# Kernel tuning notes

Measured on AMD Instinct MI355X. Metric: run time of the kernel, lower is better.

Reference implementation:

```python
import jax, jax.numpy as jnp
import numpy as np

N, E, FIN, H, FO = 50000, 800000, 256, 8, 32


def setup_inputs() -> dict:
    key = jax.random.key(0)
    ks = jax.random.split(key, 7)
    node_features = jax.random.normal(ks[0], (N, FIN), dtype=jnp.float32)
    edge_index = jax.random.randint(ks[1], (2, E), 0, N, dtype=jnp.int32).astype(jnp.int64)
    # parameters (xavier-ish scaling)
    Wp = jax.random.normal(ks[2], (H * FO, FIN), dtype=jnp.float32) * (1.0 / np.sqrt(FIN))
    a_src = jax.random.normal(ks[3], (1, H, FO), dtype=jnp.float32) * 0.1
    a_trg = jax.random.normal(ks[4], (1, H, FO), dtype=jnp.float32) * 0.1
    Wskip = jax.random.normal(ks[5], (H * FO, FIN), dtype=jnp.float32) * (1.0 / np.sqrt(FIN))
    bias = jnp.zeros((H * FO,), dtype=jnp.float32)
    return {"node_features": node_features, "edge_index": edge_index,
            "Wp": Wp, "a_src": a_src, "a_trg": a_trg, "Wskip": Wskip, "bias": bias}


def reference(node_features, edge_index, Wp, a_src, a_trg, Wskip, bias):
    # dropout is identity at inference
    x = node_features                                   # [N, FIN]
    src, trg = edge_index[0], edge_index[1]             # [E], [E]
    proj = (x @ Wp.T).reshape(-1, H, FO)                # [N, H, FO]
    scores_src = jnp.sum(proj * a_src, axis=-1)         # [N, H]
    scores_trg = jnp.sum(proj * a_trg, axis=-1)         # [N, H]
    # lift to edges
    s = scores_src[src] + scores_trg[trg]               # [E, H]
    s = jax.nn.leaky_relu(s, negative_slope=0.2)
    # global max subtraction (matches torch code: scores.max())
    s = s - jnp.max(s)
    exp_s = jnp.exp(s)                                  # [E, H]
    denom = jax.ops.segment_sum(exp_s, trg, num_segments=N)   # [N, H]
    attn = exp_s / (denom[trg] + 1e-16)                 # [E, H]
    weighted = proj[src] * attn[:, :, None]             # [E, H, FO]
    out = jax.ops.segment_sum(weighted, trg, num_segments=N)  # [N, H, FO]
    # skip connection: FO != FIN, so use skip_proj
    out = out + (x @ Wskip.T).reshape(-1, H, FO)
    out = out.reshape(-1, H * FO) + bias                # concat heads
    return jax.nn.elu(out)
```

## Files before the change

### kernel.cpp

```cpp
#include <hip/hip_runtime.h>
#include <math.h>

#define FIN 256
#define HF  256
#define NH  8

typedef __bf16 bf16x8 __attribute__((ext_vector_type(8)));
typedef float  f32x4  __attribute__((ext_vector_type(4)));

__device__ __forceinline__ unsigned short f2bf(float f) {
    unsigned u = __float_as_uint(f);
    unsigned r = (u + 0x7fffu + ((u >> 16) & 1u)) >> 16;
    return (unsigned short)r;
}
__device__ __forceinline__ float bf2f(unsigned short h) {
    return __uint_as_float(((unsigned)h) << 16);
}

__global__ __launch_bounds__(256) void convert_k(
    const float* __restrict__ x, const float* __restrict__ Wp,
    const float* __restrict__ Wskip, unsigned short* __restrict__ A2,
    unsigned short* __restrict__ W2, int M)
{
    const int l = threadIdx.x & 63;
    const int row = blockIdx.x * 4 + (threadIdx.x >> 6);
    const int total = M + 512;
    if (row >= total) return;
    const float* src;
    unsigned short* dst;
    if (row < M) { src = x + (size_t)row * 256; dst = A2 + (size_t)row * 512; }
    else {
        int j = row - M;
        src = (j < 256) ? Wp + (size_t)j * 256 : Wskip + (size_t)(j - 256) * 256;
        dst = W2 + (size_t)j * 512;
    }
    float4 v = *(const float4*)&src[l * 4];
    ushort4 h, lo;
    h.x = f2bf(v.x); lo.x = f2bf(v.x - bf2f(h.x));
    h.y = f2bf(v.y); lo.y = f2bf(v.y - bf2f(h.y));
    h.z = f2bf(v.z); lo.z = f2bf(v.z - bf2f(h.z));
    h.w = f2bf(v.w); lo.w = f2bf(v.w - bf2f(h.w));
    *(ushort4*)&dst[l * 4]       = h;
    *(ushort4*)&dst[256 + l * 4] = lo;
}

__device__ __forceinline__ void gload16(const void* g, void* l) {
    __builtin_amdgcn_global_load_lds(
        (const __attribute__((address_space(1))) void*)g,
        (__attribute__((address_space(3))) void*)l, 16, 0, 0);
}

__global__ __launch_bounds__(256) void mfma_gemm(
    const unsigned short* __restrict__ A2, const unsigned short* __restrict__ W2,
    const float* __restrict__ bias, float* __restrict__ proj,
    float* __restrict__ out, int M)
{
    __shared__ __align__(16) unsigned short sAh[8192], sAl[8192], sBh[8192], sBl[8192];

    const int tid = threadIdx.x;
    const int l   = tid & 63;
    const int w   = tid >> 6;
    const int wr  = w >> 1, wc = w & 1;
    const int brow = blockIdx.x * 128;
    const int bcol = blockIdx.y * 128;

    f32x4 acc[4][4];
    #pragma unroll
    for (int a = 0; a < 4; ++a)
        #pragma unroll
        for (int b = 0; b < 4; ++b) acc[a][b] = (f32x4){0.f, 0.f, 0.f, 0.f};

    const int srow = l >> 3;
    const int sseg = (l & 7) ^ srow;

    for (int kk = 0; kk < 4; ++kk) {
        #pragma unroll
        for (int i = 0; i < 4; ++i) {
            const int rl  = w * 32 + i * 8 + srow;
            const int lds = (w * 32 + i * 8) * 64;
            int ga = brow + rl; if (ga >= M) ga = M - 1;
            const unsigned short* gA = A2 + (size_t)ga * 512 + kk * 64 + sseg * 8;
            const unsigned short* gB = W2 + (size_t)(bcol + rl) * 512 + kk * 64 + sseg * 8;
            gload16(gA,       &sAh[lds]);
            gload16(gA + 256, &sAl[lds]);
            gload16(gB,       &sBh[lds]);
            gload16(gB + 256, &sBl[lds]);
        }
        __syncthreads();

        #pragma unroll
        for (int ks = 0; ks < 2; ++ks) {
            const int sg = ((ks * 4) + (l >> 4)) ^ (l & 7);
            bf16x8 ah[4], al[4], bh[4], bl[4];
            #pragma unroll
            for (int f = 0; f < 4; ++f) {
                const int ra = wr * 64 + f * 16 + (l & 15);
                const int rb = wc * 64 + f * 16 + (l & 15);
                ah[f] = *(const bf16x8*)&sAh[ra * 64 + sg * 8];
                al[f] = *(const bf16x8*)&sAl[ra * 64 + sg * 8];
                bh[f] = *(const bf16x8*)&sBh[rb * 64 + sg * 8];
                bl[f] = *(const bf16x8*)&sBl[rb * 64 + sg * 8];
            }
            #pragma unroll
            for (int fm = 0; fm < 4; ++fm)
                #pragma unroll
                for (int fn = 0; fn < 4; ++fn) {
                    acc[fm][fn] = __builtin_amdgcn_mfma_f32_16x16x32_bf16(ah[fm], bh[fn], acc[fm][fn], 0, 0, 0);
                    acc[fm][fn] = __builtin_amdgcn_mfma_f32_16x16x32_bf16(ah[fm], bl[fn], acc[fm][fn], 0, 0, 0);
                    acc[fm][fn] = __builtin_amdgcn_mfma_f32_16x16x32_bf16(al[fm], bh[fn], acc[fm][fn], 0, 0, 0);
                }
        }
        __syncthreads();
    }

    const bool isProj = (bcol < 256);
    #pragma unroll
    for (int fn = 0; fn < 4; ++fn) {
        const int col = bcol + wc * 64 + fn * 16 + (l & 15);
        const float bv = isProj ? 0.f : bias[col - 256];
        float* dst = isProj ? (proj + col) : (out + (col - 256));
        #pragma unroll
        for (int fm = 0; fm < 4; ++fm) {
            const int r0 = brow + wr * 64 + fm * 16 + (l >> 4) * 4;
            #pragma unroll
            for (int q = 0; q < 4; ++q) {
                const int row = r0 + q;
                if (row < M) dst[(size_t)row * 256] = acc[fm][fn][q] + bv;
            }
        }
    }
}

__global__ __launch_bounds__(256) void scores_k(
    const float* __restrict__ proj, const float* __restrict__ a_src,
    const float* __restrict__ a_trg, float* __restrict__ ssrc,
    float* __restrict__ strg, int N)
{
    const int lane = threadIdx.x & 63;
    const int node = blockIdx.x * 4 + (threadIdx.x >> 6);
    if (node >= N) return;
    float4 p  = *(const float4*)&proj[(size_t)node * HF + lane * 4];
    float4 as = *(const float4*)&a_src[lane * 4];
    float4 at = *(const float4*)&a_trg[lane * 4];
    float ps = p.x * as.x + p.y * as.y + p.z * as.z + p.w * as.w;
    float pt = p.x * at.x + p.y * at.y + p.z * at.z + p.w * at.w;
    #pragma unroll
    for (int off = 1; off < 8; off <<= 1) {
        ps += __shfl_xor(ps, off, 64);
        pt += __shfl_xor(pt, off, 64);
    }
    if ((lane & 7) == 0) {
        ssrc[node * NH + (lane >> 3)] = ps;
        strg[node * NH + (lane >> 3)] = pt;
    }
}

__device__ __forceinline__ float lrelu(float v) { return v > 0.f ? v : 0.2f * v; }

__global__ __launch_bounds__(256) void hist_k(
    const int* __restrict__ ei, int* __restrict__ deg, int E)
{
    int gid = blockIdx.x * 256 + threadIdx.x;
    int stride = gridDim.x * 256;
    for (int e = gid; e < E; e += stride)
        atomicAdd(&deg[ei[(size_t)E + e]], 1);
}

__global__ __launch_bounds__(256) void scan1_k(
    const int* __restrict__ deg, int* __restrict__ rp, int* __restrict__ bsum, int N)
{
    __shared__ int sh[256];
    const int tid = threadIdx.x;
    const int base = blockIdx.x * 4096 + tid * 16;
    int v[16], pre[16];
    int s = 0;
    #pragma unroll
    for (int i = 0; i < 16; ++i) {
        int idx = base + i;
        v[i] = (idx < N) ? deg[idx] : 0;
        pre[i] = s; s += v[i];
    }
    sh[tid] = s;
    __syncthreads();
    #pragma unroll
    for (int off = 1; off < 256; off <<= 1) {
        int t = (tid >= off) ? sh[tid - off] : 0;
        __syncthreads();
        sh[tid] += t;
        __syncthreads();
    }
    int texcl = sh[tid] - s;
    #pragma unroll
    for (int i = 0; i < 16; ++i) {
        int idx = base + i;
        if (idx < N) rp[idx] = texcl + pre[i];
    }
    if (tid == 255) bsum[blockIdx.x] = sh[255];
}

__global__ void scan2_k(int* bsum, int nsb) {
    if (threadIdx.x == 0 && blockIdx.x == 0) {
        int s = 0;
        for (int b = 0; b < nsb; ++b) { int v = bsum[b]; bsum[b] = s; s += v; }
    }
}

__global__ __launch_bounds__(256) void scan3_k(
    int* __restrict__ rp, const int* __restrict__ bsum,
    int* __restrict__ cursor, int N, int E)
{
    int gid = blockIdx.x * 256 + threadIdx.x;
    if (gid < N) {
        int v = rp[gid] + bsum[gid >> 12];
        rp[gid] = v;
        cursor[gid] = v;
    }
    if (gid == 0) rp[N] = E;
}

__global__ __launch_bounds__(256) void scatter_k(
    const int* __restrict__ ei, int* __restrict__ cursor,
    int* __restrict__ col, int E)
{
    int gid = blockIdx.x * 256 + threadIdx.x;
    int stride = gridDim.x * 256;
    for (int e = gid; e < E; e += stride) {
        int s = ei[e];
        int t = ei[(size_t)E + e];
        int pos = atomicAdd(&cursor[t], 1);
        col[pos] = s;
    }
}

__global__ __launch_bounds__(256) void gather_k(
    const int* __restrict__ rp, const int* __restrict__ col,
    const float* __restrict__ ssrc, const float* __restrict__ strg,
    const float* __restrict__ proj, float* __restrict__ out, int N)
{
    const int lane = threadIdx.x & 63;
    const int node = blockIdx.x * 4 + (threadIdx.x >> 6);
    if (node >= N) return;
    const int h = lane >> 3;

    const float st = strg[(size_t)node * NH + h];
    const int beg = rp[node], end = rp[node + 1];

    float ax = 0.f, ay = 0.f, az = 0.f, aw = 0.f, den = 0.f;

    for (int i0 = beg; i0 < end; i0 += 64) {
        int ci = (i0 + lane < end) ? col[i0 + lane] : 0;
        int cnt = end - i0; if (cnt > 64) cnt = 64;
        for (int k = 0; k < cnt; ++k) {
            int s = __shfl(ci, k, 64);
            float sv = lrelu(ssrc[(size_t)s * NH + h] + st);
            float es = __expf(sv);
            float4 p = *(const float4*)&proj[(size_t)s * HF + lane * 4];
            ax += p.x * es; ay += p.y * es; az += p.z * es; aw += p.w * es;
            den += es;
        }
    }

    const float inv = 1.f / (den + 1e-16f);
    float4 sk = *(const float4*)&out[(size_t)node * HF + lane * 4];
    float4 v;
    v.x = ax * inv + sk.x;
    v.y = ay * inv + sk.y;
    v.z = az * inv + sk.z;
    v.w = aw * inv + sk.w;
    v.x = v.x > 0.f ? v.x : expm1f(v.x);
    v.y = v.y > 0.f ? v.y : expm1f(v.y);
    v.z = v.z > 0.f ? v.z : expm1f(v.z);
    v.w = v.w > 0.f ? v.w : expm1f(v.w);
    *(float4*)&out[(size_t)node * HF + lane * 4] = v;
}

extern "C" void kernel_launch(void* const* d_in, const int* in_sizes, int n_in,
                              void* d_out, int out_size, void* d_ws, size_t ws_size,
                              hipStream_t stream) {
    const float* x     = (const float*)d_in[0];
    const int*   ei    = (const int*)d_in[1];
    const float* Wp    = (const float*)d_in[2];
    const float* a_src = (const float*)d_in[3];
    const float* a_trg = (const float*)d_in[4];
    const float* Wskip = (const float*)d_in[5];
    const float* bias  = (const float*)d_in[6];
    float* out = (float*)d_out;

    const int N = in_sizes[0] / FIN;
    const int E = in_sizes[1] / 2;
    const int nsb = (N + 4095) / 4096;

    float* proj          = (float*)d_ws;
    float* ssrc          = proj + (size_t)N * HF;
    float* strg          = ssrc + (size_t)N * NH;
    unsigned short* A2   = (unsigned short*)(strg + (size_t)N * NH);
    unsigned short* W2   = A2 + (size_t)N * 512;
    int* deg             = (int*)(W2 + 512 * 512);
    int* rp              = deg + N;
    int* cursor          = rp + (N + 1);
    int* bsum            = cursor + N;
    int* col             = bsum + 16;

    hipMemsetAsync(deg, 0, (size_t)N * sizeof(int), stream);

    convert_k<<<(N + 512 + 3) / 4, 256, 0, stream>>>(x, Wp, Wskip, A2, W2, N);

    dim3 ggrid((N + 127) / 128, 4);
    mfma_gemm<<<ggrid, 256, 0, stream>>>(A2, W2, bias, proj, out, N);

    scores_k<<<(N + 3) / 4, 256, 0, stream>>>(proj, a_src, a_trg, ssrc, strg, N);

    hist_k<<<1024, 256, 0, stream>>>(ei, deg, E);

    scan1_k<<<nsb, 256, 0, stream>>>(deg, rp, bsum, N);
    scan2_k<<<1, 64, 0, stream>>>(bsum, nsb);
    scan3_k<<<(N + 255) / 256, 256, 0, stream>>>(rp, bsum, cursor, N, E);

    scatter_k<<<1024, 256, 0, stream>>>(ei, cursor, col, E);

    gather_k<<<(N + 3) / 4, 256, 0, stream>>>(rp, col, ssrc, strg, proj, out, N);
}
```

Measured before the change: 423.0 us.

## Fuse attention scores into GEMM epilogue and store projection as bf16

The GEMM epilogue now computes the per-head source and target attention scores directly from the fp32 accumulators using cross-lane shuffles. This removes the separate scores kernel and its full re-read of the projection. The projection is written as bf16, which halves the random-gather traffic in the aggregation kernel, and that kernel's inner loop is unrolled by two to keep more loads in flight. The cost is bf16 rounding of the projected features that get aggregated, plus narrower 2-byte scattered stores in the epilogue.

```diff
diff --git a/kernel.cpp b/kernel.cpp
--- a/kernel.cpp
+++ b/kernel.cpp
@@ -52,7 +52,9 @@
 
 __global__ __launch_bounds__(256) void mfma_gemm(
     const unsigned short* __restrict__ A2, const unsigned short* __restrict__ W2,
-    const float* __restrict__ bias, float* __restrict__ proj,
+    const float* __restrict__ bias, const float* __restrict__ a_src,
+    const float* __restrict__ a_trg, unsigned short* __restrict__ projb,
+    float* __restrict__ ssrc, float* __restrict__ strg,
     float* __restrict__ out, int M)
 {
     __shared__ __align__(16) unsigned short sAh[8192], sAl[8192], sBh[8192], sBl[8192];
@@ -113,45 +115,71 @@
         __syncthreads();
     }
 
-    const bool isProj = (bcol < 256);
-    #pragma unroll
-    for (int fn = 0; fn < 4; ++fn) {
-        const int col = bcol + wc * 64 + fn * 16 + (l & 15);
-        const float bv = isProj ? 0.f : bias[col - 256];
-        float* dst = isProj ? (proj + col) : (out + (col - 256));
+    if (bcol < 256) {
+        float as[4], at[4];
+        #pragma unroll
+        for (int fn = 0; fn < 4; ++fn) {
+            const int col = bcol + wc * 64 + fn * 16 + (l & 15);
+            as[fn] = a_src[col];
+            at[fn] = a_trg[col];
+        }
+        #pragma unroll
+        for (int fn = 0; fn < 4; ++fn) {
+            const int col = bcol + wc * 64 + fn * 16 + (l & 15);
+            #pragma unroll
+            for (int fm = 0; fm < 4; ++fm) {
+                const int r0 = brow + wr * 64 + fm * 16 + (l >> 4) * 4;
+                #pragma unroll
+                for (int q = 0; q < 4; ++q) {
+                    const int row = r0 + q;
+                    if (row < M) projb[(size_t)row * 256 + col] = f2bf(acc[fm][fn][q]);
+                }
+            }
+        }
+        const int headA = ((bcol + wc * 64) >> 5);
+        const int headB = headA + 1;
         #pragma unroll
         for (int fm = 0; fm < 4; ++fm) {
-            const int r0 = brow + wr * 64 + fm * 16 + (l >> 4) * 4;
             #pragma unroll
             for (int q = 0; q < 4; ++q) {
-                const int row = r0 + q;
-                if (row < M) dst[(size_t)row * 256] = acc[fm][fn][q] + bv;
+                float p0 = acc[fm][0][q] * as[0] + acc[fm][1][q] * as[1];
+                float p1 = acc[fm][2][q] * as[2] + acc[fm][3][q] * as[3];
+                float t0 = acc[fm][0][q] * at[0] + acc[fm][1][q] * at[1];
+                float t1 = acc[fm][2][q] * at[2] + acc[fm][3][q] * at[3];
+                #pragma unroll
+                for (int m = 1; m < 16; m <<= 1) {
+                    p0 += __shfl_xor(p0, m, 64);
+                    p1 += __shfl_xor(p1, m, 64);
+                    t0 += __shfl_xor(t0, m, 64);
+                    t1 += __shfl_xor(t1, m, 64);
+                }
+                if ((l & 15) == 0) {
+                    const int row = brow + wr * 64 + fm * 16 + (l >> 4) * 4 + q;
+                    if (row < M) {
+                        ssrc[(size_t)row * NH + headA] = p0;
+                        ssrc[(size_t)row * NH + headB] = p1;
+                        strg[(size_t)row * NH + headA] = t0;
+                        strg[(size_t)row * NH + headB] = t1;
+                    }
+                }
             }
         }
-    }
-}
-
-__global__ __launch_bounds__(256) void scores_k(
-    const float* __restrict__ proj, const float* __restrict__ a_src,
-    const float* __restrict__ a_trg, float* __restrict__ ssrc,
-    float* __restrict__ strg, int N)
-{
-    const int lane = threadIdx.x & 63;
-    const int node = blockIdx.x * 4 + (threadIdx.x >> 6);
-    if (node >= N) return;
-    float4 p  = *(const float4*)&proj[(size_t)node * HF + lane * 4];
-    float4 as = *(const float4*)&a_src[lane * 4];
-    float4 at = *(const float4*)&a_trg[lane * 4];
-    float ps = p.x * as.x + p.y * as.y + p.z * as.z + p.w * as.w;
-    float pt = p.x * at.x + p.y * at.y + p.z * at.z + p.w * at.w;
-    #pragma unroll
-    for (int off = 1; off < 8; off <<= 1) {
-        ps += __shfl_xor(ps, off, 64);
-        pt += __shfl_xor(pt, off, 64);
-    }
-    if ((lane & 7) == 0) {
-        ssrc[node * NH + (lane >> 3)] = ps;
-        strg[node * NH + (lane >> 3)] = pt;
+    } else {
+        #pragma unroll
+        for (int fn = 0; fn < 4; ++fn) {
+            const int col = bcol + wc * 64 + fn * 16 + (l & 15);
+            const float bv = bias[col - 256];
+            float* dst = out + (col - 256);
+            #pragma unroll
+            for (int fm = 0; fm < 4; ++fm) {
+                const int r0 = brow + wr * 64 + fm * 16 + (l >> 4) * 4;
+                #pragma unroll
+                for (int q = 0; q < 4; ++q) {
+                    const int row = r0 + q;
+                    if (row < M) dst[(size_t)row * 256] = acc[fm][fn][q] + bv;
+                }
+            }
+        }
     }
 }
 
@@ -235,7 +263,7 @@
 __global__ __launch_bounds__(256) void gather_k(
     const int* __restrict__ rp, const int* __restrict__ col,
     const float* __restrict__ ssrc, const float* __restrict__ strg,
-    const float* __restrict__ proj, float* __restrict__ out, int N)
+    const unsigned short* __restrict__ projb, float* __restrict__ out, int N)
 {
     const int lane = threadIdx.x & 63;
     const int node = blockIdx.x * 4 + (threadIdx.x >> 6);
@@ -250,13 +278,29 @@
     for (int i0 = beg; i0 < end; i0 += 64) {
         int ci = (i0 + lane < end) ? col[i0 + lane] : 0;
         int cnt = end - i0; if (cnt > 64) cnt = 64;
-        for (int k = 0; k < cnt; ++k) {
-            int s = __shfl(ci, k, 64);
-            float sv = lrelu(ssrc[(size_t)s * NH + h] + st);
-            float es = __expf(sv);
-            float4 p = *(const float4*)&proj[(size_t)s * HF + lane * 4];
-            ax += p.x * es; ay += p.y * es; az += p.z * es; aw += p.w * es;
-            den += es;
+        int k = 0;
+        for (; k + 1 < cnt; k += 2) {
+            int s0 = __shfl(ci, k, 64);
+            int s1 = __shfl(ci, k + 1, 64);
+            ushort4 r0 = *(const ushort4*)&projb[(size_t)s0 * HF + lane * 4];
+            ushort4 r1 = *(const ushort4*)&projb[(size_t)s1 * HF + lane * 4];
+            float e0 = __expf(lrelu(ssrc[(size_t)s0 * NH + h] + st));
+            float e1 = __expf(lrelu(ssrc[(size_t)s1 * NH + h] + st));
+            ax += bf2f(r0.x) * e0 + bf2f(r1.x) * e1;
+            ay += bf2f(r0.y) * e0 + bf2f(r1.y) * e1;
+            az += bf2f(r0.z) * e0 + bf2f(r1.z) * e1;
+            aw += bf2f(r0.w) * e0 + bf2f(r1.w) * e1;
+            den += e0 + e1;
+        }
+        if (k < cnt) {
+            int s0 = __shfl(ci, k, 64);
+            ushort4 r0 = *(const ushort4*)&projb[(size_t)s0 * HF + lane * 4];
+            float e0 = __expf(lrelu(ssrc[(size_t)s0 * NH + h] + st));
+            ax += bf2f(r0.x) * e0;
+            ay += bf2f(r0.y) * e0;
+            az += bf2f(r0.z) * e0;
+            aw += bf2f(r0.w) * e0;
+            den += e0;
         }
     }
 
@@ -290,8 +334,8 @@
     const int E = in_sizes[1] / 2;
     const int nsb = (N + 4095) / 4096;
 
-    float* proj          = (float*)d_ws;
-    float* ssrc          = proj + (size_t)N * HF;
+    unsigned short* projb = (unsigned short*)d_ws;
+    float* ssrc          = (float*)(projb + (size_t)N * HF);
     float* strg          = ssrc + (size_t)N * NH;
     unsigned short* A2   = (unsigned short*)(strg + (size_t)N * NH);
     unsigned short* W2   = A2 + (size_t)N * 512;
@@ -306,9 +350,8 @@
     convert_k<<<(N + 512 + 3) / 4, 256, 0, stream>>>(x, Wp, Wskip, A2, W2, N);
 
     dim3 ggrid((N + 127) / 128, 4);
-    mfma_gemm<<<ggrid, 256, 0, stream>>>(A2, W2, bias, proj, out, N);
-
-    scores_k<<<(N + 3) / 4, 256, 0, stream>>>(proj, a_src, a_trg, ssrc, strg, N);
+    mfma_gemm<<<ggrid, 256, 0, stream>>>(A2, W2, bias, a_src, a_trg,
+                                         projb, ssrc, strg, out, N);
 
     hist_k<<<1024, 256, 0, stream>>>(ei, deg, E);
 
@@ -318,5 +361,5 @@
 
     scatter_k<<<1024, 256, 0, stream>>>(ei, cursor, col, E);
 
-    gather_k<<<(N + 3) / 4, 256, 0, stream>>>(rp, col, ssrc, strg, proj, out, N);
-}
+    gather_k<<<(N + 3) / 4, 256, 0, stream>>>(rp, col, ssrc, strg, projb, out, N);
+}
```

New measurement: 367.6 us. 13.1% less time.
